# Kernel tuning notes

Measured on AMD Instinct MI355X. Metric: run time of the kernel, lower is better.

## Reference

```python
import jax, jax.numpy as jnp
import numpy as np
import math

SEQ_LEN, PRED_LEN, CHANNELS, RANK = 720, 336, 862, 32
IN_LEN = SEQ_LEN // 2  # Haar low-pass with stride 2 (seq_len even)
BATCH = 256


def _dct2_ortho_mat(N):
    # D[k, n] = s_k * 2 * cos(pi * k * (2n+1) / (2N)); orthonormal DCT-II
    k = np.arange(N)[:, None]
    n = np.arange(N)[None, :]
    D = 2.0 * np.cos(np.pi * k * (2 * n + 1) / (2 * N))
    s = np.full(N, np.sqrt(1.0 / (2 * N)))
    s[0] = np.sqrt(1.0 / (4 * N))
    return jnp.asarray((s[:, None] * D).astype(np.float32))


def _idct2_unnorm_mat(N):
    # scipy.fft.idct(type=2, norm=None): out[n] = (1/N) * (x0/2 + sum_{k>=1} x_k cos(pi k (2n+1)/(2N)))
    # Returned as M[k, n] so that out = x @ M along last axis.
    k = np.arange(N)[:, None]
    n = np.arange(N)[None, :]
    M = np.cos(np.pi * k * (2 * n + 1) / (2 * N)) / N
    M[0, :] *= 0.5
    return jnp.asarray(M.astype(np.float32))


D_DCT = _dct2_ortho_mat(IN_LEN)        # [IN_LEN, IN_LEN]
M_IDCT = _idct2_unnorm_mat(PRED_LEN)   # [PRED_LEN, PRED_LEN]
INV_SQRT2 = 1.0 / math.sqrt(2.0)


def setup_inputs() -> dict:
    key = jax.random.key(0)
    k1, k2, k3, k4 = jax.random.split(key, 4)
    x = jax.random.normal(k1, (BATCH, SEQ_LEN, CHANNELS), dtype=jnp.float32)
    # kaiming_uniform-like scales for LowRank params
    boundA = math.sqrt(6.0 / IN_LEN)
    boundB = math.sqrt(6.0 / RANK)
    A = jax.random.uniform(k2, (IN_LEN, RANK), dtype=jnp.float32, minval=-boundA, maxval=boundA)
    B = jax.random.uniform(k3, (RANK, PRED_LEN), dtype=jnp.float32, minval=-boundB, maxval=boundB)
    b = jax.random.uniform(k4, (PRED_LEN,), dtype=jnp.float32)
    return {"x": x, "A": A, "B": B, "b": b}


def reference(x, A, B, b):
    # x: [B, L, C] -> [B, C, L]
    xt = jnp.transpose(x, (0, 2, 1))
    seq_mean = jnp.mean(xt, axis=-1, keepdims=True)          # [B, C, 1]
    xc = xt - seq_mean
    # Haar low-pass: depthwise conv1d with [1,1]/sqrt(2), stride 2
    h = (xc[..., ::2] + xc[..., 1::2]) * INV_SQRT2           # [B, C, IN_LEN]
    # orthonormal DCT-II along last axis, then divide by length
    y = jnp.einsum('bcn,kn->bck', h, D_DCT) / IN_LEN         # [B, C, IN_LEN]
    # low-rank prediction head (shared across channels)
    z = (y @ A) @ B + b                                      # [B, C, PRED_LEN]
    # unnormalized inverse DCT-II (scipy idct type=2, norm=None)
    o = z @ M_IDCT                                           # [B, C, PRED_LEN]
    o = o + seq_mean
    return jnp.transpose(o, (0, 2, 1))                       # [B, PRED_LEN, C]
```

## Files before the change

kernel.cpp:

```cpp
#include <hip/hip_runtime.h>
#include <math.h>

#define SEQ_LEN   720
#define IN_LEN    360
#define PRED_LEN  336
#define CHANNELS  862
#define RANK      32
#define BATCH     256

typedef _Float16 h2 __attribute__((ext_vector_type(2)));

#define WS_WP    0
#define WS_VT    11520
#define WS_CVEC  22272
#define WS_WH    22608
#define WS_VH    28368

#define L_EX     0
#define L_W      29376
#define L_V      35136
#define L_CV     40512

__device__ __forceinline__ float fdot2w(h2 a, h2 b, float c) {
#if __has_builtin(__builtin_amdgcn_fdot2)
    return __builtin_amdgcn_fdot2(a, b, c, false);
#else
    return fmaf((float)a[0], (float)b[0], fmaf((float)a[1], (float)b[1], c));
#endif
}
__device__ __forceinline__ h2 pkrtz(float a, float b) {
    return __builtin_bit_cast(h2, __builtin_amdgcn_cvt_pkrtz(a, b));
}
#define BC(u)  __builtin_bit_cast(h2, (u))
#define BCU(v) __builtin_bit_cast(unsigned, (v))

__global__ __launch_bounds__(256) void k_prep(const float* __restrict__ A,
                                              const float* __restrict__ B,
                                              const float* __restrict__ bias,
                                              float* __restrict__ Wp,
                                              float* __restrict__ Vt,
                                              float* __restrict__ cvec) {
    __shared__ float sbuf[IN_LEN * RANK];
    int blk = blockIdx.x;
    if (blk < 45) {
        for (int i = threadIdx.x; i < IN_LEN * RANK; i += 256) sbuf[i] = A[i];
        __syncthreads();
        int idx = blk * 256 + threadIdx.x;
        int n = idx >> 5, r = idx & 31;
        int step = 2 * n + 1, m = 0;
        float sum = 0.f;
        for (int k = 0; k < IN_LEN; ++k) {
            float coef = (k == 0) ? 0.05270462766947299f
                                  : 0.07453559924999299f;
            float d = coef * cospif((float)m * (1.0f / 720.0f));
            sum = fmaf(d, sbuf[k * RANK + r], sum);
            m += step; if (m >= 1440) m -= 1440;
        }
        Wp[idx] = sum * 0.0019641855032960957f;
    } else if (blk < 87) {
        for (int i = threadIdx.x; i < PRED_LEN * RANK; i += 256) {
            int r = i / PRED_LEN, k = i - r * PRED_LEN;
            sbuf[k * RANK + r] = B[i];
        }
        __syncthreads();
        int idx = (blk - 45) * 256 + threadIdx.x;
        int n = idx >> 5, r = idx & 31;
        int step = 2 * n + 1, m = 0;
        float sum = 0.f;
        for (int k = 0; k < PRED_LEN; ++k) {
            float mk = cospif((float)m * (1.0f / 672.0f));
            if (k == 0) mk *= 0.5f;
            sum = fmaf(mk, sbuf[k * RANK + r], sum);
            m += step; if (m >= 1344) m -= 1344;
        }
        Vt[idx] = sum * (1.0f / 336.0f);
    } else {
        int n = (blk - 87) * 256 + threadIdx.x;
        if (n < PRED_LEN) {
            int step = 2 * n + 1, m = 0;
            float sum = 0.f;
            for (int k = 0; k < PRED_LEN; ++k) {
                float mk = cospif((float)m * (1.0f / 672.0f));
                if (k == 0) mk *= 0.5f;
                sum = fmaf(mk, bias[k], sum);
                m += step; if (m >= 1344) m -= 1344;
            }
            cvec[n] = sum * (1.0f / 336.0f);
        }
    }
}

__global__ __launch_bounds__(256) void k_pack(const float* __restrict__ Wp,
                                              const float* __restrict__ Vt,
                                              unsigned* __restrict__ Wh,
                                              unsigned* __restrict__ Vh) {
    int idx = blockIdx.x * 256 + threadIdx.x;
    if (idx < 5760) {
        int n = idx >> 4, j = idx & 15;
        h2 v = pkrtz(Wp[n * RANK + 2 * j], Wp[n * RANK + 2 * j + 1]);
        Wh[idx] = BCU(v);
    } else if (idx < 5760 + 5376) {
        int k = idx - 5760;
        int n = k >> 4, j = k & 15;
        h2 v = pkrtz(Vt[n * RANK + 2 * j], Vt[n * RANK + 2 * j + 1]);
        Vh[k] = BCU(v);
    }
}

__global__ __launch_bounds__(512) void k_main(const float* __restrict__ x,
                                              const float* __restrict__ A,
                                              const unsigned* __restrict__ Wh,
                                              const unsigned* __restrict__ Vh,
                                              const float* __restrict__ cvec,
                                              float* __restrict__ out) {
    __shared__ unsigned ldsu[40848];
    const int tid = threadIdx.x;
    const int b = blockIdx.x;
    const int h = tid >> 8;
    const int i = tid & 255;
    const bool active = (i < 216);
    const int c0 = (i < 215) ? 4 * i : 858;

    for (int idx = tid; idx < 1440; idx += 512)
        ((uint4*)(ldsu + L_W))[idx] = ((const uint4*)Wh)[idx];
    for (int idx = tid; idx < 1344; idx += 512)
        ((uint4*)(ldsu + L_V))[idx] = ((const uint4*)Vh)[idx];
    for (int idx = tid; idx < 84; idx += 512)
        ((uint4*)(ldsu + L_CV))[idx] = ((const uint4*)cvec)[idx];
    __syncthreads();

    h2 acc0[16], acc1[16], acc2[16], acc3[16];
    #pragma unroll
    for (int j = 0; j < 16; ++j) {
        acc0[j] = pkrtz(0.f, 0.f); acc1[j] = pkrtz(0.f, 0.f);
        acc2[j] = pkrtz(0.f, 0.f); acc3[j] = pkrtz(0.f, 0.f);
    }
    float S0 = 0.f, S1 = 0.f, S2 = 0.f, S3 = 0.f;

    if (active) {
        const float* xp = x + (size_t)b * (SEQ_LEN * CHANNELS)
                            + (size_t)h * (IN_LEN * CHANNELS) + c0;
        float2 bA[4], bB[4];
        #define LOADN(BUF, NL) { const float* p_ = xp + (size_t)(2 * (NL)) * CHANNELS; \
            BUF[0] = *(const float2*)(p_);                 \
            BUF[1] = *(const float2*)(p_ + 2);             \
            BUF[2] = *(const float2*)(p_ + CHANNELS);      \
            BUF[3] = *(const float2*)(p_ + CHANNELS + 2); }

        #define BODY(BUF, NL) { \
            float p0 = BUF[0].x + BUF[2].x; \
            float p1 = BUF[0].y + BUF[2].y; \
            float p2 = BUF[1].x + BUF[3].x; \
            float p3 = BUF[1].y + BUF[3].y; \
            S0 += p0; S1 += p1; S2 += p2; S3 += p3; \
            h2 P0 = pkrtz(p0, p0), P1 = pkrtz(p1, p1); \
            h2 P2 = pkrtz(p2, p2), P3 = pkrtz(p3, p3); \
            const uint4* wr = (const uint4*)(ldsu + L_W) + ((NL) + 180 * h) * 4; \
            _Pragma("unroll") \
            for (int q_ = 0; q_ < 4; ++q_) { \
                uint4 wv = wr[q_]; \
                h2 w0 = BC(wv.x), w1 = BC(wv.y), w2 = BC(wv.z), w3 = BC(wv.w); \
                acc0[4*q_+0] = w0 * P0 + acc0[4*q_+0]; \
                acc1[4*q_+0] = w0 * P1 + acc1[4*q_+0]; \
                acc2[4*q_+0] = w0 * P2 + acc2[4*q_+0]; \
                acc3[4*q_+0] = w0 * P3 + acc3[4*q_+0]; \
                acc0[4*q_+1] = w1 * P0 + acc0[4*q_+1]; \
                acc1[4*q_+1] = w1 * P1 + acc1[4*q_+1]; \
                acc2[4*q_+1] = w1 * P2 + acc2[4*q_+1]; \
                acc3[4*q_+1] = w1 * P3 + acc3[4*q_+1]; \
                acc0[4*q_+2] = w2 * P0 + acc0[4*q_+2]; \
                acc1[4*q_+2] = w2 * P1 + acc1[4*q_+2]; \
                acc2[4*q_+2] = w2 * P2 + acc2[4*q_+2]; \
                acc3[4*q_+2] = w2 * P3 + acc3[4*q_+2]; \
                acc0[4*q_+3] = w3 * P0 + acc0[4*q_+3]; \
                acc1[4*q_+3] = w3 * P1 + acc1[4*q_+3]; \
                acc2[4*q_+3] = w3 * P2 + acc2[4*q_+3]; \
                acc3[4*q_+3] = w3 * P3 + acc3[4*q_+3]; \
            } }

        LOADN(bA, 0)
        for (int n = 0; n < 180; n += 2) {
            LOADN(bB, n + 1)
            BODY(bA, n)
            if (n + 2 < 180) LOADN(bA, n + 2)
            BODY(bB, n + 1)
        }
        #undef BODY
        #undef LOADN
    }

    if (active) {
        uint4* rec = (uint4*)(ldsu + (i + 216 * h) * 68);
        #pragma unroll
        for (int q = 0; q < 4; ++q) {
            uint4 v;
            v.x = BCU(acc0[4*q+0]); v.y = BCU(acc0[4*q+1]);
            v.z = BCU(acc0[4*q+2]); v.w = BCU(acc0[4*q+3]);
            rec[q] = v;
            v.x = BCU(acc1[4*q+0]); v.y = BCU(acc1[4*q+1]);
            v.z = BCU(acc1[4*q+2]); v.w = BCU(acc1[4*q+3]);
            rec[4 + q] = v;
            v.x = BCU(acc2[4*q+0]); v.y = BCU(acc2[4*q+1]);
            v.z = BCU(acc2[4*q+2]); v.w = BCU(acc2[4*q+3]);
            rec[8 + q] = v;
            v.x = BCU(acc3[4*q+0]); v.y = BCU(acc3[4*q+1]);
            v.z = BCU(acc3[4*q+2]); v.w = BCU(acc3[4*q+3]);
            rec[12 + q] = v;
        }
        uint4 sv;
        sv.x = __float_as_uint(S0); sv.y = __float_as_uint(S1);
        sv.z = __float_as_uint(S2); sv.w = __float_as_uint(S3);
        rec[16] = sv;
    }
    __syncthreads();

    float mean0 = 0.f, mean1 = 0.f, mean2 = 0.f, mean3 = 0.f;
    if (active) {
        const uint4* pr = (const uint4*)(ldsu + (i + 216 * (1 - h)) * 68);
        #pragma unroll
        for (int q = 0; q < 4; ++q) {
            uint4 v = pr[q];
            acc0[4*q+0] = acc0[4*q+0] + BC(v.x); acc0[4*q+1] = acc0[4*q+1] + BC(v.y);
            acc0[4*q+2] = acc0[4*q+2] + BC(v.z); acc0[4*q+3] = acc0[4*q+3] + BC(v.w);
            v = pr[4 + q];
            acc1[4*q+0] = acc1[4*q+0] + BC(v.x); acc1[4*q+1] = acc1[4*q+1] + BC(v.y);
            acc1[4*q+2] = acc1[4*q+2] + BC(v.z); acc1[4*q+3] = acc1[4*q+3] + BC(v.w);
            v = pr[8 + q];
            acc2[4*q+0] = acc2[4*q+0] + BC(v.x); acc2[4*q+1] = acc2[4*q+1] + BC(v.y);
            acc2[4*q+2] = acc2[4*q+2] + BC(v.z); acc2[4*q+3] = acc2[4*q+3] + BC(v.w);
            v = pr[12 + q];
            acc3[4*q+0] = acc3[4*q+0] + BC(v.x); acc3[4*q+1] = acc3[4*q+1] + BC(v.y);
            acc3[4*q+2] = acc3[4*q+2] + BC(v.z); acc3[4*q+3] = acc3[4*q+3] + BC(v.w);
        }
        uint4 sv = pr[16];
        S0 += __uint_as_float(sv.x); S1 += __uint_as_float(sv.y);
        S2 += __uint_as_float(sv.z); S3 += __uint_as_float(sv.w);

        const float kc = (1.0f / 360.0f) * 0.037267799624996496f;
        float g0 = -S0 * kc, g1 = -S1 * kc, g2 = -S2 * kc, g3 = -S3 * kc;
        h2 G0 = pkrtz(g0, g0), G1 = pkrtz(g1, g1), G2 = pkrtz(g2, g2), G3 = pkrtz(g3, g3);
        #pragma unroll
        for (int q = 0; q < 8; ++q) {
            float4 a4 = ((const float4*)A)[q];
            h2 aa = pkrtz(a4.x, a4.y), ab = pkrtz(a4.z, a4.w);
            acc0[2*q]   = aa * G0 + acc0[2*q];   acc0[2*q+1] = ab * G0 + acc0[2*q+1];
            acc1[2*q]   = aa * G1 + acc1[2*q];   acc1[2*q+1] = ab * G1 + acc1[2*q+1];
            acc2[2*q]   = aa * G2 + acc2[2*q];   acc2[2*q+1] = ab * G2 + acc2[2*q+1];
            acc3[2*q]   = aa * G3 + acc3[2*q];   acc3[2*q+1] = ab * G3 + acc3[2*q+1];
        }
        mean0 = S0 * (1.0f / 720.0f); mean1 = S1 * (1.0f / 720.0f);
        mean2 = S2 * (1.0f / 720.0f); mean3 = S3 * (1.0f / 720.0f);

        float* op = out + (size_t)b * (PRED_LEN * CHANNELS)
                        + (size_t)(168 * h) * CHANNELS + c0;
        for (int nl = 0; nl < 168; ++nl) {
            const int n = 168 * h + nl;
            const uint4* vr = (const uint4*)(ldsu + L_V) + n * 4;
            float o0 = 0.f, o1 = 0.f, o2 = 0.f, o3 = 0.f;
            float e0 = 0.f, e1 = 0.f, e2 = 0.f, e3 = 0.f;
            #pragma unroll
            for (int q = 0; q < 4; ++q) {
                uint4 v = vr[q];
                h2 v0 = BC(v.x), v1 = BC(v.y), v2 = BC(v.z), v3 = BC(v.w);
                o0 = fdot2w(acc0[4*q+0], v0, o0); e0 = fdot2w(acc0[4*q+1], v1, e0);
                o1 = fdot2w(acc1[4*q+0], v0, o1); e1 = fdot2w(acc1[4*q+1], v1, e1);
                o2 = fdot2w(acc2[4*q+0], v0, o2); e2 = fdot2w(acc2[4*q+1], v1, e2);
                o3 = fdot2w(acc3[4*q+0], v0, o3); e3 = fdot2w(acc3[4*q+1], v1, e3);
                o0 = fdot2w(acc0[4*q+2], v2, o0); e0 = fdot2w(acc0[4*q+3], v3, e0);
                o1 = fdot2w(acc1[4*q+2], v2, o1); e1 = fdot2w(acc1[4*q+3], v3, e1);
                o2 = fdot2w(acc2[4*q+2], v2, o2); e2 = fdot2w(acc2[4*q+3], v3, e2);
                o3 = fdot2w(acc3[4*q+2], v2, o3); e3 = fdot2w(acc3[4*q+3], v3, e3);
            }
            float cvn = ((const float*)(ldsu + L_CV))[n];
            float2 w0, w1;
            w0.x = (o0 + e0) + cvn + mean0;
            w0.y = (o1 + e1) + cvn + mean1;
            w1.x = (o2 + e2) + cvn + mean2;
            w1.y = (o3 + e3) + cvn + mean3;
            *(float2*)(op)     = w0;
            *(float2*)(op + 2) = w1;
            op += CHANNELS;
        }
    }
}


extern "C" void kernel_launch(void* const* d_in, const int* in_sizes, int n_in,
                              void* d_out, int out_size, void* d_ws, size_t ws_size,
                              hipStream_t stream) {
    (void)in_sizes; (void)n_in; (void)out_size; (void)ws_size;
    const float* x    = (const float*)d_in[0];
    const float* A    = (const float*)d_in[1];
    const float* B    = (const float*)d_in[2];
    const float* bias = (const float*)d_in[3];
    float* out = (float*)d_out;
    float* ws  = (float*)d_ws;

    float*    Wp   = ws + WS_WP;
    float*    Vt   = ws + WS_VT;
    float*    cvec = ws + WS_CVEC;
    unsigned* Wh   = (unsigned*)(ws + WS_WH);
    unsigned* Vh   = (unsigned*)(ws + WS_VH);

    k_prep<<<dim3(89), dim3(256), 0, stream>>>(A, B, bias, Wp, Vt, cvec);
    k_pack<<<dim3(44), dim3(256), 0, stream>>>(Wp, Vt, Wh, Vh);
    k_main<<<dim3(BATCH), dim3(512), 0, stream>>>(x, A, Wh, Vh, cvec, out);
}
```

Before: 271.6 us.

## Fuse pack into prep, deepen x-load prefetch, use nontemporal output stores

The fp16 packing step moves into k_prep through a shared-memory staging buffer, which removes the k_pack launch and the fp32 intermediate workspace. The main loop's x prefetch goes from a two-buffer to a four-buffer rotation, keeping three loads in flight ahead of compute to hide global memory latency, at the cost of more registers. Output stores become nontemporal to avoid polluting the cache with write-only data. Clamping the tail load index to 179 re-reads a valid row instead of skipping the load.

```diff
diff --git a/kernel.cpp b/kernel.cpp
--- a/kernel.cpp
+++ b/kernel.cpp
@@ -10,11 +10,9 @@
 
 typedef _Float16 h2 __attribute__((ext_vector_type(2)));
 
-#define WS_WP    0
-#define WS_VT    11520
-#define WS_CVEC  22272
-#define WS_WH    22608
-#define WS_VH    28368
+#define WS_WH    0
+#define WS_VH    5760
+#define WS_CV    11136
 
 #define L_EX     0
 #define L_W      29376
@@ -34,19 +32,25 @@
 #define BC(u)  __builtin_bit_cast(h2, (u))
 #define BCU(v) __builtin_bit_cast(unsigned, (v))
 
+__device__ __forceinline__ void ntstore2(float* p, float2 v) {
+    __builtin_nontemporal_store(__builtin_bit_cast(unsigned long long, v),
+                                (unsigned long long*)p);
+}
+
 __global__ __launch_bounds__(256) void k_prep(const float* __restrict__ A,
                                               const float* __restrict__ B,
                                               const float* __restrict__ bias,
-                                              float* __restrict__ Wp,
-                                              float* __restrict__ Vt,
+                                              unsigned* __restrict__ Wh,
+                                              unsigned* __restrict__ Vh,
                                               float* __restrict__ cvec) {
     __shared__ float sbuf[IN_LEN * RANK];
+    __shared__ float sres[256];
+    const int t = threadIdx.x;
     int blk = blockIdx.x;
     if (blk < 45) {
-        for (int i = threadIdx.x; i < IN_LEN * RANK; i += 256) sbuf[i] = A[i];
+        for (int i = t; i < IN_LEN * RANK; i += 256) sbuf[i] = A[i];
         __syncthreads();
-        int idx = blk * 256 + threadIdx.x;
-        int n = idx >> 5, r = idx & 31;
+        int n = blk * 8 + (t >> 5), r = t & 31;
         int step = 2 * n + 1, m = 0;
         float sum = 0.f;
         for (int k = 0; k < IN_LEN; ++k) {
@@ -56,15 +60,20 @@
             sum = fmaf(d, sbuf[k * RANK + r], sum);
             m += step; if (m >= 1440) m -= 1440;
         }
-        Wp[idx] = sum * 0.0019641855032960957f;
+        sres[t] = sum * 0.0019641855032960957f;
+        __syncthreads();
+        if (t < 128) {
+            int nl = t >> 4, j = t & 15;
+            h2 v = pkrtz(sres[nl * 32 + 2 * j], sres[nl * 32 + 2 * j + 1]);
+            Wh[(blk * 8 + nl) * 16 + j] = BCU(v);
+        }
     } else if (blk < 87) {
-        for (int i = threadIdx.x; i < PRED_LEN * RANK; i += 256) {
+        for (int i = t; i < PRED_LEN * RANK; i += 256) {
             int r = i / PRED_LEN, k = i - r * PRED_LEN;
             sbuf[k * RANK + r] = B[i];
         }
         __syncthreads();
-        int idx = (blk - 45) * 256 + threadIdx.x;
-        int n = idx >> 5, r = idx & 31;
+        int n = (blk - 45) * 8 + (t >> 5), r = t & 31;
         int step = 2 * n + 1, m = 0;
         float sum = 0.f;
         for (int k = 0; k < PRED_LEN; ++k) {
@@ -73,9 +82,15 @@
             sum = fmaf(mk, sbuf[k * RANK + r], sum);
             m += step; if (m >= 1344) m -= 1344;
         }
-        Vt[idx] = sum * (1.0f / 336.0f);
+        sres[t] = sum * (1.0f / 336.0f);
+        __syncthreads();
+        if (t < 128) {
+            int nl = t >> 4, j = t & 15;
+            h2 v = pkrtz(sres[nl * 32 + 2 * j], sres[nl * 32 + 2 * j + 1]);
+            Vh[((blk - 45) * 8 + nl) * 16 + j] = BCU(v);
+        }
     } else {
-        int n = (blk - 87) * 256 + threadIdx.x;
+        int n = (blk - 87) * 256 + t;
         if (n < PRED_LEN) {
             int step = 2 * n + 1, m = 0;
             float sum = 0.f;
@@ -87,23 +102,6 @@
             }
             cvec[n] = sum * (1.0f / 336.0f);
         }
-    }
-}
-
-__global__ __launch_bounds__(256) void k_pack(const float* __restrict__ Wp,
-                                              const float* __restrict__ Vt,
-                                              unsigned* __restrict__ Wh,
-                                              unsigned* __restrict__ Vh) {
-    int idx = blockIdx.x * 256 + threadIdx.x;
-    if (idx < 5760) {
-        int n = idx >> 4, j = idx & 15;
-        h2 v = pkrtz(Wp[n * RANK + 2 * j], Wp[n * RANK + 2 * j + 1]);
-        Wh[idx] = BCU(v);
-    } else if (idx < 5760 + 5376) {
-        int k = idx - 5760;
-        int n = k >> 4, j = k & 15;
-        h2 v = pkrtz(Vt[n * RANK + 2 * j], Vt[n * RANK + 2 * j + 1]);
-        Vh[k] = BCU(v);
     }
 }
 
@@ -140,7 +138,7 @@
     if (active) {
         const float* xp = x + (size_t)b * (SEQ_LEN * CHANNELS)
                             + (size_t)h * (IN_LEN * CHANNELS) + c0;
-        float2 bA[4], bB[4];
+        float2 b0[4], b1[4], b2[4], b3[4];
         #define LOADN(BUF, NL) { const float* p_ = xp + (size_t)(2 * (NL)) * CHANNELS; \
             BUF[0] = *(const float2*)(p_);                 \
             BUF[1] = *(const float2*)(p_ + 2);             \
@@ -178,12 +176,17 @@
                 acc3[4*q_+3] = w3 * P3 + acc3[4*q_+3]; \
             } }
 
-        LOADN(bA, 0)
-        for (int n = 0; n < 180; n += 2) {
-            LOADN(bB, n + 1)
-            BODY(bA, n)
-            if (n + 2 < 180) LOADN(bA, n + 2)
-            BODY(bB, n + 1)
+        LOADN(b0, 0) LOADN(b1, 1) LOADN(b2, 2)
+        for (int it = 0; it < 45; ++it) {
+            const int base = 4 * it;
+            LOADN(b3, base + 3)
+            BODY(b0, base)
+            { int nn = (base + 4 < 180) ? base + 4 : 179; LOADN(b0, nn) }
+            BODY(b1, base + 1)
+            { int nn = (base + 5 < 180) ? base + 5 : 179; LOADN(b1, nn) }
+            BODY(b2, base + 2)
+            { int nn = (base + 6 < 180) ? base + 6 : 179; LOADN(b2, nn) }
+            BODY(b3, base + 3)
         }
         #undef BODY
         #undef LOADN
@@ -214,7 +217,6 @@
     }
     __syncthreads();
 
-    float mean0 = 0.f, mean1 = 0.f, mean2 = 0.f, mean3 = 0.f;
     if (active) {
         const uint4* pr = (const uint4*)(ldsu + (i + 216 * (1 - h)) * 68);
         #pragma unroll
@@ -233,11 +235,11 @@
             acc3[4*q+2] = acc3[4*q+2] + BC(v.z); acc3[4*q+3] = acc3[4*q+3] + BC(v.w);
         }
         uint4 sv = pr[16];
-        S0 += __uint_as_float(sv.x); S1 += __uint_as_float(sv.y);
-        S2 += __uint_as_float(sv.z); S3 += __uint_as_float(sv.w);
+        float S0f = S0 + __uint_as_float(sv.x), S1f = S1 + __uint_as_float(sv.y);
+        float S2f = S2 + __uint_as_float(sv.z), S3f = S3 + __uint_as_float(sv.w);
 
         const float kc = (1.0f / 360.0f) * 0.037267799624996496f;
-        float g0 = -S0 * kc, g1 = -S1 * kc, g2 = -S2 * kc, g3 = -S3 * kc;
+        float g0 = -S0f * kc, g1 = -S1f * kc, g2 = -S2f * kc, g3 = -S3f * kc;
         h2 G0 = pkrtz(g0, g0), G1 = pkrtz(g1, g1), G2 = pkrtz(g2, g2), G3 = pkrtz(g3, g3);
         #pragma unroll
         for (int q = 0; q < 8; ++q) {
@@ -248,8 +250,8 @@
             acc2[2*q]   = aa * G2 + acc2[2*q];   acc2[2*q+1] = ab * G2 + acc2[2*q+1];
             acc3[2*q]   = aa * G3 + acc3[2*q];   acc3[2*q+1] = ab * G3 + acc3[2*q+1];
         }
-        mean0 = S0 * (1.0f / 720.0f); mean1 = S1 * (1.0f / 720.0f);
-        mean2 = S2 * (1.0f / 720.0f); mean3 = S3 * (1.0f / 720.0f);
+        const float mean0 = S0f * (1.0f / 720.0f), mean1 = S1f * (1.0f / 720.0f);
+        const float mean2 = S2f * (1.0f / 720.0f), mean3 = S3f * (1.0f / 720.0f);
 
         float* op = out + (size_t)b * (PRED_LEN * CHANNELS)
                         + (size_t)(168 * h) * CHANNELS + c0;
@@ -277,8 +279,8 @@
             w0.y = (o1 + e1) + cvn + mean1;
             w1.x = (o2 + e2) + cvn + mean2;
             w1.y = (o3 + e3) + cvn + mean3;
-            *(float2*)(op)     = w0;
-            *(float2*)(op + 2) = w1;
+            ntstore2(op,     w0);
+            ntstore2(op + 2, w1);
             op += CHANNELS;
         }
     }
@@ -294,15 +296,11 @@
     const float* B    = (const float*)d_in[2];
     const float* bias = (const float*)d_in[3];
     float* out = (float*)d_out;
-    float* ws  = (float*)d_ws;
-
-    float*    Wp   = ws + WS_WP;
-    float*    Vt   = ws + WS_VT;
-    float*    cvec = ws + WS_CVEC;
-    unsigned* Wh   = (unsigned*)(ws + WS_WH);
-    unsigned* Vh   = (unsigned*)(ws + WS_VH);
-
-    k_prep<<<dim3(89), dim3(256), 0, stream>>>(A, B, bias, Wp, Vt, cvec);
-    k_pack<<<dim3(44), dim3(256), 0, stream>>>(Wp, Vt, Wh, Vh);
+
+    unsigned* Wh   = (unsigned*)d_ws + WS_WH;
+    unsigned* Vh   = (unsigned*)d_ws + WS_VH;
+    float*    cvec = (float*)d_ws + WS_CV;
+
+    k_prep<<<dim3(89), dim3(256), 0, stream>>>(A, B, bias, Wh, Vh, cvec);
     k_main<<<dim3(BATCH), dim3(512), 0, stream>>>(x, A, Wh, Vh, cvec, out);
 }
```

After: 249.0 us. -8.3%, faster.
